# Performance work log

Measured on AMD Instinct MI355X. Metric: run time of the kernel, lower is better.

The kernel has to match this reference:

```python
import jax, jax.numpy as jnp
import numpy as np
from jax import lax

BITWIDTH = 7
EPS = 1e-5


def ti_quant(x):
    """TiFloatToInt8: per-tensor int8 quantization with power-of-2 scale."""
    rng = jnp.max(jnp.abs(x))
    bw = jnp.ceil(jnp.log2(rng))
    exp = bw - BITWIDTH
    q = jnp.clip(jnp.round(x * 2.0 ** (BITWIDTH - bw)), -128.0, 127.0)
    return q, exp


def ti_conv(xv, xe, wv, we, pad):
    """TiConv2d: integer conv (simulated in f32, all values int-valued),
    int32 accumulate, then shift back to 8 bits; exponents add."""
    acc = lax.conv_general_dilated(
        xv, wv, window_strides=(1, 1), padding=[(pad, pad), (pad, pad)],
        dimension_numbers=("NCHW", "OIHW", "NCHW"))
    rng = jnp.max(jnp.abs(acc))
    bw = jnp.ceil(jnp.log2(rng))
    shift = jnp.maximum(bw - BITWIDTH, 0.0)
    q = jnp.clip(jnp.round(acc * 2.0 ** (-shift)), -128.0, 127.0)
    return q, xe + we + shift


def batchnorm(x, gamma, beta):
    # training-mode BN: batch statistics over (N, H, W)
    mean = jnp.mean(x, axis=(0, 2, 3), keepdims=True)
    var = jnp.var(x, axis=(0, 2, 3), keepdims=True)
    g = gamma[None, :, None, None]
    b = beta[None, :, None, None]
    return g * (x - mean) * lax.rsqrt(var + EPS) + b


def setup_inputs() -> dict:
    key = jax.random.key(0)
    k0, k1, k2, k3, k4 = jax.random.split(key, 5)
    B, Cin, Cout, H, W = 32, 128, 256, 56, 56
    x_val = jax.random.randint(k0, (B, Cin, H, W), -128, 128, dtype=jnp.int32)
    x_exp = jnp.zeros((), jnp.float32) - 7.0
    wDW = jnp.round(jnp.clip(jax.random.normal(k1, (Cin, Cin, 3, 3), jnp.float32) * 32.0, -128.0, 127.0))
    wDW_exp = jnp.zeros((), jnp.float32) - 9.0
    wPW = jnp.round(jnp.clip(jax.random.normal(k2, (Cout, Cin, 1, 1), jnp.float32) * 32.0, -128.0, 127.0))
    wPW_exp = jnp.zeros((), jnp.float32) - 9.0
    gamma1 = jnp.ones((Cin,), jnp.float32) + 0.1 * jax.random.normal(k3, (Cin,), jnp.float32)
    beta1 = jnp.zeros((Cin,), jnp.float32)
    gamma2 = jnp.ones((Cout,), jnp.float32) + 0.1 * jax.random.normal(k4, (Cout,), jnp.float32)
    beta2 = jnp.zeros((Cout,), jnp.float32)
    return {"x_val": x_val, "x_exp": x_exp, "wDW": wDW, "wDW_exp": wDW_exp,
            "wPW": wPW, "wPW_exp": wPW_exp, "gamma1": gamma1, "beta1": beta1,
            "gamma2": gamma2, "beta2": beta2}


def reference(x_val, x_exp, wDW, wDW_exp, wPW, wPW_exp, gamma1, beta1, gamma2, beta2):
    xv = x_val.astype(jnp.float32)
    # convDW (3x3, in->in, pad=1)
    q, e = ti_conv(xv, x_exp, wDW, wDW_exp, 1)
    # dequant -> bn1 -> quant
    f = batchnorm(q * 2.0 ** e, gamma1, beta1)
    q, e = ti_quant(f)
    # TiReLU on int values
    q = jnp.maximum(q, 0.0)
    # convPW (1x1, in->out)
    q, e = ti_conv(q, e, wPW, wPW_exp, 0)
    # dequant -> bn2 -> quant -> relu
    f = batchnorm(q * 2.0 ** e, gamma2, beta2)
    q, e = ti_quant(f)
    q = jnp.maximum(q, 0.0)
    return q.astype(jnp.int8), e
```

## Files before the change

### kernel.cpp

```cpp
#include <hip/hip_runtime.h>
#include <cstdint>
#include <cstddef>

#define C1 128
#define C2 256
#define Hh 56
#define Wd 56
#define HW 3136
#define NHW 100352
#define N1 ((size_t)12845056)
#define N2 ((size_t)25690112)
#define XPSZ ((size_t)13778944)

typedef int v4i __attribute__((ext_vector_type(4)));
typedef int v16i __attribute__((ext_vector_type(16)));

static constexpr size_t OFF_XP = 0;
static constexpr size_t OFF_ACC1 = XPSZ;
static constexpr size_t OFF_Q1 = OFF_ACC1 + 4 * N1;
static constexpr size_t OFF_Q3 = OFF_Q1 + N1;
static constexpr size_t OFF_WQ1 = OFF_Q3 + N2;
static constexpr size_t OFF_WQ2 = OFF_WQ1 + 147456;
static constexpr size_t OFF_STATS = OFF_WQ2 + 32768;

struct Stats {
  int absmax1, absmax2, pad0, pad1;
  float scale1, e1, s2, e2;
  float scaleq2, e3, sf, ef;
  int sum1[C1]; unsigned sumsq1[C1];
  int min1[C1], max1[C1];
  float A1[C1], B1c[C1];
  int sum2[C2]; unsigned sumsq2[C2];
  int min2[C2], max2[C2];
  float A2[C2], B2c[C2];
};

__global__ void k_init(Stats* st) {
  int t = threadIdx.x;
  if (t == 0) { st->absmax1 = 0; st->absmax2 = 0; }
  for (int c = t; c < C1; c += 256) {
    st->sum1[c] = 0; st->sumsq1[c] = 0; st->min1[c] = 127; st->max1[c] = -128;
  }
  for (int c = t; c < C2; c += 256) {
    st->sum2[c] = 0; st->sumsq2[c] = 0; st->min2[c] = 127; st->max2[c] = -128;
  }
}

__global__ __launch_bounds__(256) void k_prep_x2(
    const int* __restrict__ x, signed char* __restrict__ xp) {
  __shared__ signed char lds[56 * 132];
  int t = threadIdx.x;
  int hh = blockIdx.x;
  int n = blockIdx.y;
  int* xpw = (int*)(xp + ((size_t)n * 58 + hh) * 7424);
  if (hh == 0 || hh == 57) {
    for (int o = t; o < 1856; o += 256) xpw[o] = 0;
    return;
  }
  int h = hh - 1;
  const int* xb = x + (size_t)n * C1 * HW + h * 56;
  for (int idx = t; idx < 7168; idx += 256) {
    int c = idx / 56, w = idx - c * 56;
    lds[w * 132 + c] = (signed char)xb[(size_t)c * HW + w];
  }
  __syncthreads();
  for (int o = t; o < 1856; o += 256) {
    int kb = o / 232, r = o - kb * 232, ww = r >> 2, cw = r & 3;
    int val = (ww == 0 || ww == 57) ? 0
              : *(const int*)&lds[(ww - 1) * 132 + kb * 16 + cw * 4];
    xpw[o] = val;
  }
}

__global__ void k_prep_w1(const float* __restrict__ wDW, signed char* __restrict__ wq1t) {
  int idx = blockIdx.x * 256 + threadIdx.x;
  if (idx >= 128 * 1152) return;
  int co = idx / 1152, r = idx - co * 1152;
  int ci = r / 9, pos = r - ci * 9;
  int k = pos * 128 + ci;
  wq1t[(size_t)(k >> 4) * 2048 + co * 16 + (k & 15)] = (signed char)(int)wDW[idx];
}

__global__ void k_prep_w2(const float* __restrict__ wPW, signed char* __restrict__ wq2t) {
  int i = blockIdx.x * 256 + threadIdx.x;
  int co = i >> 7, ci = i & 127;
  wq2t[(size_t)(ci >> 4) * 4096 + co * 16 + (ci & 15)] = (signed char)(int)wPW[i];
}

__device__ inline v4i ld16_lds(const signed char* p) {
  const int2* q = (const int2*)p;
  int2 lo = q[0], hi = q[1];
  v4i r; r[0] = lo.x; r[1] = lo.y; r[2] = hi.x; r[3] = hi.y;
  return r;
}

__global__ __launch_bounds__(256, 2) void k_conv1s(
    const signed char* __restrict__ xp, const signed char* __restrict__ wq1t,
    int* __restrict__ acc1, Stats* st) {
  __shared__ int reda[4];
  int t = threadIdx.x, lane = t & 63, wave = t >> 6;
  int half = lane >> 5, l31 = lane & 31;
  size_t g0 = (size_t)blockIdx.x * 256;

  const signed char* ab[2];
#pragma unroll
  for (int i = 0; i < 2; ++i) {
    size_t gm = g0 + wave * 64 + i * 32 + l31;
    int n = (int)(gm / HW);
    int p = (int)(gm - (size_t)n * HW);
    int h = p / 56, w = p - h * 56;
    ab[i] = xp + ((size_t)n * 58 + h) * 7424 + w * 16 + half * 928;
  }
  const signed char* bb[4];
#pragma unroll
  for (int j = 0; j < 4; ++j)
    bb[j] = wq1t + (size_t)(j * 32 + l31) * 16 + half * 2048;

  v16i a1[2][4];
#pragma unroll
  for (int i = 0; i < 2; ++i)
#pragma unroll
    for (int j = 0; j < 4; ++j)
#pragma unroll
      for (int r = 0; r < 16; ++r) a1[i][j][r] = 0;

#pragma unroll
  for (int pos = 0; pos < 9; ++pos) {
    int kh = pos / 3, kw = pos - kh * 3;
    const signed char* a0p = ab[0] + kh * 7424 + kw * 16;
    const signed char* a1p = ab[1] + kh * 7424 + kw * 16;
#pragma unroll
    for (int kb = 0; kb < 8; kb += 2) {
      v4i af0 = *(const v4i*)(a0p + kb * 928);
      v4i af1 = *(const v4i*)(a1p + kb * 928);
      v4i bf[4];
#pragma unroll
      for (int j = 0; j < 4; ++j)
        bf[j] = *(const v4i*)(bb[j] + pos * 16384 + kb * 2048);
#pragma unroll
      for (int j = 0; j < 4; ++j) {
        a1[0][j] = __builtin_amdgcn_mfma_i32_32x32x32_i8(af0, bf[j], a1[0][j], 0, 0, 0);
        a1[1][j] = __builtin_amdgcn_mfma_i32_32x32x32_i8(af1, bf[j], a1[1][j], 0, 0, 0);
      }
    }
  }

  int am = 0;
#pragma unroll
  for (int i = 0; i < 2; ++i)
#pragma unroll
    for (int j = 0; j < 4; ++j)
#pragma unroll
      for (int r = 0; r < 16; ++r) am = max(am, abs(a1[i][j][r]));
  for (int off = 32; off; off >>= 1) am = max(am, __shfl_down(am, off, 64));
  if (lane == 0) reda[wave] = am;
  __syncthreads();
  if (t == 0)
    atomicMax(&st->absmax1, max(max(reda[0], reda[1]), max(reda[2], reda[3])));

  int* ob = acc1 + (size_t)blockIdx.x * 32768;
#pragma unroll
  for (int i = 0; i < 2; ++i)
#pragma unroll
    for (int j = 0; j < 4; ++j)
#pragma unroll
      for (int reg = 0; reg < 16; ++reg)
        ob[(((wave * 2 + i) * 4 + j) * 16 + reg) * 64 + lane] = a1[i][j][reg];
}

__global__ __launch_bounds__(256, 2) void k_qstats1(
    const int* __restrict__ acc1, signed char* __restrict__ q1, Stats* st,
    const float* __restrict__ x_exp, const float* __restrict__ wDW_exp) {
  __shared__ int qti[256 * 34];
  __shared__ int psum[C1], psq[C1], pmn[C1], pmx[C1];
  signed char* qt = (signed char*)qti;
  int t = threadIdx.x, lane = t & 63, wave = t >> 6;
  int half = lane >> 5, l31 = lane & 31;

  if (t < C1) { psum[t] = 0; psq[t] = 0; pmn[t] = 127; pmx[t] = -128; }
  __syncthreads();

  int v1 = st->absmax1;
  int pw = 31 - __clz(v1 | 1);
  int bw = ((v1 & (v1 - 1)) == 0) ? pw : pw + 1;
  int sh = max(bw - 7, 0);
  float scale1 = exp2f((float)(-sh));
  if (blockIdx.x == 0 && t == 0)
    st->e1 = x_exp[0] + wDW_exp[0] + (float)sh;

  const int* ib = acc1 + (size_t)blockIdx.x * 32768;
#pragma unroll
  for (int j = 0; j < 4; ++j) {
    int sj = 0, sqj = 0, mnj = 127, mxj = -128;
    int c = j * 32 + l31;
#pragma unroll
    for (int i = 0; i < 2; ++i)
#pragma unroll
      for (int reg = 0; reg < 16; ++reg) {
        int av = ib[(((wave * 2 + i) * 4 + j) * 16 + reg) * 64 + lane];
        int row = (reg & 3) + 8 * (reg >> 2) + 4 * half;
        int pix = wave * 64 + i * 32 + row;
        float r = rintf((float)av * scale1);
        r = fminf(fmaxf(r, -128.f), 127.f);
        int qi = (int)r;
        qt[pix * 136 + c] = (signed char)qi;
        sj += qi; sqj += qi * qi; mnj = min(mnj, qi); mxj = max(mxj, qi);
      }
    sj += __shfl_down(sj, 32, 64);
    sqj += __shfl_down(sqj, 32, 64);
    mnj = min(mnj, __shfl_down(mnj, 32, 64));
    mxj = max(mxj, __shfl_down(mxj, 32, 64));
    if (half == 0) {
      atomicAdd(&psum[c], sj); atomicAdd(&psq[c], sqj);
      atomicMin(&pmn[c], mnj); atomicMax(&pmx[c], mxj);
    }
  }
  __syncthreads();
  if (t < C1) {
    atomicAdd(&st->sum1[t], psum[t]);
    atomicAdd(&st->sumsq1[t], (unsigned)psq[t]);
    atomicMin(&st->min1[t], pmn[t]);
    atomicMax(&st->max1[t], pmx[t]);
  }
  int* q1w = (int*)(q1 + (size_t)blockIdx.x * 256 * 128);
  for (int idx = t; idx < 8192; idx += 256) {
    int pix = idx >> 5, c4 = idx & 31;
    q1w[idx] = qti[pix * 34 + c4];
  }
}

template <int STORE>
__global__ __launch_bounds__(256, 2) void k_conv2t(
    const signed char* __restrict__ q1, const signed char* __restrict__ wq2t,
    signed char* __restrict__ q3, Stats* st, const float* __restrict__ wPW_exp) {
  __shared__ int qti[128 * 34];
  __shared__ signed char stg[128 * 264];
  __shared__ int psum[C2], psq[C2], pmn[C2], pmx[C2];
  __shared__ int reda[4];
  signed char* qt = (signed char*)qti;

  int t = threadIdx.x, lane = t & 63, wave = t >> 6;
  int half = lane >> 5, l31 = lane & 31;
  size_t g0 = (size_t)blockIdx.x * 128;

  if (STORE) { psum[t] = 0; psq[t] = 0; pmn[t] = 127; pmx[t] = -128; }

  int c4 = t & 31;
  float Av[4], Bv[4];
#pragma unroll
  for (int jj = 0; jj < 4; ++jj) {
    Av[jj] = st->A1[c4 * 4 + jj];
    Bv[jj] = st->B1c[c4 * 4 + jj];
  }
  float s2 = st->s2;
  const int* q1w = (const int*)(q1 + g0 * 128);
#pragma unroll
  for (int k = 0; k < 16; ++k) {
    int idx = k * 256 + t;
    int v = q1w[idx];
    int pix = idx >> 5;
    int outv = 0;
#pragma unroll
    for (int jj = 0; jj < 4; ++jj) {
      int b = (signed char)(v >> (8 * jj));
      float y = Av[jj] * (float)b + Bv[jj];
      float r = rintf(y * s2);
      r = fminf(fmaxf(r, -128.f), 127.f);
      r = fmaxf(r, 0.f);
      outv |= ((int)r & 0xff) << (8 * jj);
    }
    qti[pix * 34 + c4] = outv;
  }
  __syncthreads();

  v16i acc[8];
#pragma unroll
  for (int j = 0; j < 8; ++j)
#pragma unroll
    for (int r = 0; r < 16; ++r) acc[j][r] = 0;

#pragma unroll
  for (int ks = 0; ks < 4; ++ks) {
    v4i af = ld16_lds(&qt[(wave * 32 + l31) * 136 + half * 16 + ks * 32]);
#pragma unroll
    for (int j = 0; j < 8; ++j) {
      v4i bf = *(const v4i*)(wq2t + (size_t)(ks * 2 + half) * 4096 + (j * 32 + l31) * 16);
      acc[j] = __builtin_amdgcn_mfma_i32_32x32x32_i8(af, bf, acc[j], 0, 0, 0);
    }
  }

  if (STORE == 0) {
    int am2 = 0;
#pragma unroll
    for (int j = 0; j < 8; ++j)
#pragma unroll
      for (int r = 0; r < 16; ++r) am2 = max(am2, abs(acc[j][r]));
    for (int off = 32; off; off >>= 1) am2 = max(am2, __shfl_down(am2, off, 64));
    if (lane == 0) reda[wave] = am2;
    __syncthreads();
    if (t == 0)
      atomicMax(&st->absmax2, max(max(reda[0], reda[1]), max(reda[2], reda[3])));
  } else {
    int v2 = st->absmax2;
    int pw = 31 - __clz(v2 | 1);
    int bw = ((v2 & (v2 - 1)) == 0) ? pw : pw + 1;
    int sh2 = max(bw - 7, 0);
    float scale2 = exp2f((float)(-sh2));
    if (blockIdx.x == 0 && t == 0)
      st->e3 = st->e2 + wPW_exp[0] + (float)sh2;
#pragma unroll
    for (int j = 0; j < 8; ++j) {
      int c = j * 32 + l31;
      int sj = 0, sqj = 0, mnj = 127, mxj = -128;
#pragma unroll
      for (int reg = 0; reg < 16; ++reg) {
        int row = (reg & 3) + 8 * (reg >> 2) + 4 * half;
        float r = rintf((float)acc[j][reg] * scale2);
        r = fminf(fmaxf(r, -128.f), 127.f);
        int qi = (int)r;
        stg[(wave * 32 + row) * 264 + c] = (signed char)qi;
        sj += qi; sqj += qi * qi; mnj = min(mnj, qi); mxj = max(mxj, qi);
      }
      sj += __shfl_down(sj, 32, 64);
      sqj += __shfl_down(sqj, 32, 64);
      mnj = min(mnj, __shfl_down(mnj, 32, 64));
      mxj = max(mxj, __shfl_down(mxj, 32, 64));
      if (half == 0) {
        atomicAdd(&psum[c], sj); atomicAdd(&psq[c], sqj);
        atomicMin(&pmn[c], mnj); atomicMax(&pmx[c], mxj);
      }
    }
    __syncthreads();
    atomicAdd(&st->sum2[t], psum[t]);
    atomicAdd(&st->sumsq2[t], (unsigned)psq[t]);
    atomicMin(&st->min2[t], pmn[t]);
    atomicMax(&st->max2[t], pmx[t]);
    int* q3w = (int*)(q3 + g0 * 256);
#pragma unroll
    for (int k = 0; k < 32; ++k) {
      int idx = k * 256 + t;
      int pix = idx >> 6, cw = idx & 63;
      q3w[idx] = *(const int*)&stg[pix * 264 + cw * 4];
    }
  }
}

__global__ void k_bn(const int* __restrict__ sums,
                     const unsigned* __restrict__ sumsqs,
                     const int* __restrict__ mins, const int* __restrict__ maxs,
                     const float* __restrict__ gamma, const float* __restrict__ beta,
                     const float* __restrict__ e_in,
                     float* A, float* Bc, float* s_out, float* e_out,
                     float* e_extra, int C) {
  __shared__ float red[4];
  int t = threadIdx.x;
  float e1 = *e_in;
  double meanq = (double)sums[t] / (double)NHW;
  double varq = (double)sumsqs[t] / (double)NHW - meanq * meanq;
  float se = exp2f(e1);
  float mean = (float)meanq * se;
  float var = (float)varq * se * se;
  float rsq = 1.0f / sqrtf(var + 1e-5f);
  float g = gamma[t], b = beta[t];
  float Avv = g * se * rsq;
  float Bvv = b - g * mean * rsq;
  A[t] = Avv; Bc[t] = Bvv;
  float cand = fmaxf(fabsf(Avv * (float)mins[t] + Bvv), fabsf(Avv * (float)maxs[t] + Bvv));
  for (int off = 32; off; off >>= 1) cand = fmaxf(cand, __shfl_down(cand, off, 64));
  int wave = t >> 6, lane = t & 63;
  if (lane == 0) red[wave] = cand;
  __syncthreads();
  if (t == 0) {
    float rng = red[0];
    for (int i = 1; i < C / 64; i++) rng = fmaxf(rng, red[i]);
    float bwv = ceilf(log2f(rng));
    *s_out = exp2f(7.0f - bwv);
    *e_out = bwv - 7.0f;
    if (e_extra) *e_extra = bwv - 7.0f;
  }
}

__global__ __launch_bounds__(256) void k_out(
    const signed char* __restrict__ q3, const Stats* __restrict__ st,
    float* __restrict__ out) {
  __shared__ signed char lds[64 * 260];
  int t = threadIdx.x, lane = t & 63, wave = t >> 6;
  size_t g0 = (size_t)blockIdx.x * 64;
  int n = (int)(g0 / HW), p0 = (int)(g0 - (size_t)n * HW);
  const int* q3w = (const int*)(q3 + g0 * 256);
#pragma unroll
  for (int k = 0; k < 16; ++k) {
    int idx = k * 256 + t;
    int pix = idx >> 6, cw = idx & 63;
    *(int*)&lds[pix * 260 + cw * 4] = q3w[idx];
  }
  __syncthreads();
  float sf = st->sf;
  float* ob = out + (size_t)n * C2 * HW + p0 + lane;
#pragma unroll
  for (int cg = 0; cg < 16; ++cg) {
    int v = *(const int*)&lds[lane * 260 + wave * 64 + cg * 4];
#pragma unroll
    for (int jj = 0; jj < 4; ++jj) {
      int c = wave * 64 + cg * 4 + jj;
      float y = st->A2[c] * (float)((signed char)(v >> (8 * jj))) + st->B2c[c];
      float r = rintf(y * sf);
      r = fminf(fmaxf(r, -128.f), 127.f);
      ob[(size_t)c * HW] = fmaxf(r, 0.f);
    }
  }
}

extern "C" void kernel_launch(void* const* d_in, const int* in_sizes, int n_in,
                              void* d_out, int out_size, void* d_ws, size_t ws_size,
                              hipStream_t stream) {
  const int* x = (const int*)d_in[0];
  const float* x_exp = (const float*)d_in[1];
  const float* wDW = (const float*)d_in[2];
  const float* wDW_exp = (const float*)d_in[3];
  const float* wPW = (const float*)d_in[4];
  const float* wPW_exp = (const float*)d_in[5];
  const float* gamma1 = (const float*)d_in[6];
  const float* beta1 = (const float*)d_in[7];
  const float* gamma2 = (const float*)d_in[8];
  const float* beta2 = (const float*)d_in[9];
  float* out = (float*)d_out;

  char* ws = (char*)d_ws;
  signed char* xp2 = (signed char*)(ws + OFF_XP);
  int* acc1 = (int*)(ws + OFF_ACC1);
  signed char* q1 = (signed char*)(ws + OFF_Q1);
  signed char* q3 = (signed char*)(ws + OFF_Q3);
  signed char* wq1t = (signed char*)(ws + OFF_WQ1);
  signed char* wq2t = (signed char*)(ws + OFF_WQ2);
  Stats* st = (Stats*)(ws + OFF_STATS);

  hipLaunchKernelGGL(k_init, dim3(1), dim3(256), 0, stream, st);
  hipLaunchKernelGGL(k_prep_x2, dim3(58, 32), dim3(256), 0, stream, x, xp2);
  hipLaunchKernelGGL(k_prep_w1, dim3(576), dim3(256), 0, stream, wDW, wq1t);
  hipLaunchKernelGGL(k_prep_w2, dim3(128), dim3(256), 0, stream, wPW, wq2t);

  hipLaunchKernelGGL(k_conv1s, dim3(392), dim3(256), 0, stream,
                     xp2, wq1t, acc1, st);
  hipLaunchKernelGGL(k_qstats1, dim3(392), dim3(256), 0, stream,
                     acc1, q1, st, x_exp, wDW_exp);
  hipLaunchKernelGGL(k_bn, dim3(1), dim3(C1), 0, stream,
                     st->sum1, st->sumsq1, st->min1, st->max1, gamma1, beta1,
                     &st->e1, st->A1, st->B1c, &st->s2, &st->e2, (float*)nullptr, C1);

  hipLaunchKernelGGL(k_conv2t<0>, dim3(784), dim3(256), 0, stream,
                     q1, wq2t, q3, st, wPW_exp);
  hipLaunchKernelGGL(k_conv2t<1>, dim3(784), dim3(256), 0, stream,
                     q1, wq2t, q3, st, wPW_exp);
  hipLaunchKernelGGL(k_bn, dim3(1), dim3(C2), 0, stream,
                     st->sum2, st->sumsq2, st->min2, st->max2, gamma2, beta2,
                     &st->e3, st->A2, st->B2c, &st->sf, &st->ef, out + N2, C2);
  hipLaunchKernelGGL(k_out, dim3(1568), dim3(256), 0, stream, q3, st, out);
}
```

Measured before the change: 297.7 us.

## Fold BN-parameter kernels into consumers, merge prep kernels, halve conv1 tiles

```diff
diff --git a/kernel.cpp b/kernel.cpp
--- a/kernel.cpp
+++ b/kernel.cpp
@@ -29,20 +29,32 @@
   float scaleq2, e3, sf, ef;
   int sum1[C1]; unsigned sumsq1[C1];
   int min1[C1], max1[C1];
-  float A1[C1], B1c[C1];
   int sum2[C2]; unsigned sumsq2[C2];
   int min2[C2], max2[C2];
-  float A2[C2], B2c[C2];
 };
 
-__global__ void k_init(Stats* st) {
-  int t = threadIdx.x;
-  if (t == 0) { st->absmax1 = 0; st->absmax2 = 0; }
-  for (int c = t; c < C1; c += 256) {
-    st->sum1[c] = 0; st->sumsq1[c] = 0; st->min1[c] = 127; st->max1[c] = -128;
-  }
-  for (int c = t; c < C2; c += 256) {
-    st->sum2[c] = 0; st->sumsq2[c] = 0; st->min2[c] = 127; st->max2[c] = -128;
+__global__ __launch_bounds__(256) void k_prep_all(
+    const float* __restrict__ wDW, const float* __restrict__ wPW,
+    signed char* __restrict__ wq1t, signed char* __restrict__ wq2t, Stats* st) {
+  int b = blockIdx.x, t = threadIdx.x;
+  if (b < 576) {
+    int idx = b * 256 + t;
+    int co = idx / 1152, r = idx - co * 1152;
+    int ci = r / 9, pos = r - ci * 9;
+    int k = pos * 128 + ci;
+    wq1t[(size_t)(k >> 4) * 2048 + co * 16 + (k & 15)] = (signed char)(int)wDW[idx];
+  } else if (b < 704) {
+    int i = (b - 576) * 256 + t;
+    int co = i >> 7, ci = i & 127;
+    wq2t[(size_t)(ci >> 4) * 4096 + co * 16 + (ci & 15)] = (signed char)(int)wPW[i];
+  } else {
+    if (t == 0) { st->absmax1 = 0; st->absmax2 = 0; }
+    for (int c = t; c < C1; c += 256) {
+      st->sum1[c] = 0; st->sumsq1[c] = 0; st->min1[c] = 127; st->max1[c] = -128;
+    }
+    for (int c = t; c < C2; c += 256) {
+      st->sum2[c] = 0; st->sumsq2[c] = 0; st->min2[c] = 127; st->max2[c] = -128;
+    }
   }
 }
 
@@ -72,21 +84,6 @@
   }
 }
 
-__global__ void k_prep_w1(const float* __restrict__ wDW, signed char* __restrict__ wq1t) {
-  int idx = blockIdx.x * 256 + threadIdx.x;
-  if (idx >= 128 * 1152) return;
-  int co = idx / 1152, r = idx - co * 1152;
-  int ci = r / 9, pos = r - ci * 9;
-  int k = pos * 128 + ci;
-  wq1t[(size_t)(k >> 4) * 2048 + co * 16 + (k & 15)] = (signed char)(int)wDW[idx];
-}
-
-__global__ void k_prep_w2(const float* __restrict__ wPW, signed char* __restrict__ wq2t) {
-  int i = blockIdx.x * 256 + threadIdx.x;
-  int co = i >> 7, ci = i & 127;
-  wq2t[(size_t)(ci >> 4) * 4096 + co * 16 + (ci & 15)] = (signed char)(int)wPW[i];
-}
-
 __device__ inline v4i ld16_lds(const signed char* p) {
   const int2* q = (const int2*)p;
   int2 lo = q[0], hi = q[1];
@@ -94,33 +91,34 @@
   return r;
 }
 
-__global__ __launch_bounds__(256, 2) void k_conv1s(
+__global__ __launch_bounds__(256, 4) void k_conv1s(
     const signed char* __restrict__ xp, const signed char* __restrict__ wq1t,
     int* __restrict__ acc1, Stats* st) {
   __shared__ int reda[4];
   int t = threadIdx.x, lane = t & 63, wave = t >> 6;
   int half = lane >> 5, l31 = lane & 31;
-  size_t g0 = (size_t)blockIdx.x * 256;
+  int mw = wave & 1, nw = wave >> 1;
+  size_t g0 = (size_t)blockIdx.x * 128;
 
   const signed char* ab[2];
 #pragma unroll
   for (int i = 0; i < 2; ++i) {
-    size_t gm = g0 + wave * 64 + i * 32 + l31;
+    size_t gm = g0 + mw * 64 + i * 32 + l31;
     int n = (int)(gm / HW);
     int p = (int)(gm - (size_t)n * HW);
     int h = p / 56, w = p - h * 56;
     ab[i] = xp + ((size_t)n * 58 + h) * 7424 + w * 16 + half * 928;
   }
-  const signed char* bb[4];
-#pragma unroll
-  for (int j = 0; j < 4; ++j)
-    bb[j] = wq1t + (size_t)(j * 32 + l31) * 16 + half * 2048;
-
-  v16i a1[2][4];
+  const signed char* bb[2];
+#pragma unroll
+  for (int j = 0; j < 2; ++j)
+    bb[j] = wq1t + (size_t)(nw * 64 + j * 32 + l31) * 16 + half * 2048;
+
+  v16i a1[2][2];
 #pragma unroll
   for (int i = 0; i < 2; ++i)
 #pragma unroll
-    for (int j = 0; j < 4; ++j)
+    for (int j = 0; j < 2; ++j)
 #pragma unroll
       for (int r = 0; r < 16; ++r) a1[i][j][r] = 0;
 
@@ -133,15 +131,12 @@
     for (int kb = 0; kb < 8; kb += 2) {
       v4i af0 = *(const v4i*)(a0p + kb * 928);
       v4i af1 = *(const v4i*)(a1p + kb * 928);
-      v4i bf[4];
-#pragma unroll
-      for (int j = 0; j < 4; ++j)
-        bf[j] = *(const v4i*)(bb[j] + pos * 16384 + kb * 2048);
-#pragma unroll
-      for (int j = 0; j < 4; ++j) {
-        a1[0][j] = __builtin_amdgcn_mfma_i32_32x32x32_i8(af0, bf[j], a1[0][j], 0, 0, 0);
-        a1[1][j] = __builtin_amdgcn_mfma_i32_32x32x32_i8(af1, bf[j], a1[1][j], 0, 0, 0);
-      }
+      v4i bf0 = *(const v4i*)(bb[0] + pos * 16384 + kb * 2048);
+      v4i bf1 = *(const v4i*)(bb[1] + pos * 16384 + kb * 2048);
+      a1[0][0] = __builtin_amdgcn_mfma_i32_32x32x32_i8(af0, bf0, a1[0][0], 0, 0, 0);
+      a1[0][1] = __builtin_amdgcn_mfma_i32_32x32x32_i8(af0, bf1, a1[0][1], 0, 0, 0);
+      a1[1][0] = __builtin_amdgcn_mfma_i32_32x32x32_i8(af1, bf0, a1[1][0], 0, 0, 0);
+      a1[1][1] = __builtin_amdgcn_mfma_i32_32x32x32_i8(af1, bf1, a1[1][1], 0, 0, 0);
     }
   }
 
@@ -149,7 +144,7 @@
 #pragma unroll
   for (int i = 0; i < 2; ++i)
 #pragma unroll
-    for (int j = 0; j < 4; ++j)
+    for (int j = 0; j < 2; ++j)
 #pragma unroll
       for (int r = 0; r < 16; ++r) am = max(am, abs(a1[i][j][r]));
   for (int off = 32; off; off >>= 1) am = max(am, __shfl_down(am, off, 64));
@@ -158,24 +153,25 @@
   if (t == 0)
     atomicMax(&st->absmax1, max(max(reda[0], reda[1]), max(reda[2], reda[3])));
 
-  int* ob = acc1 + (size_t)blockIdx.x * 32768;
+  int* ob = acc1 + (size_t)blockIdx.x * 16384;
 #pragma unroll
   for (int i = 0; i < 2; ++i)
 #pragma unroll
-    for (int j = 0; j < 4; ++j)
+    for (int j = 0; j < 2; ++j)
 #pragma unroll
       for (int reg = 0; reg < 16; ++reg)
-        ob[(((wave * 2 + i) * 4 + j) * 16 + reg) * 64 + lane] = a1[i][j][reg];
-}
-
-__global__ __launch_bounds__(256, 2) void k_qstats1(
+        ob[(((wave * 2 + i) * 2 + j) * 16 + reg) * 64 + lane] = a1[i][j][reg];
+}
+
+__global__ __launch_bounds__(256, 4) void k_qstats1(
     const int* __restrict__ acc1, signed char* __restrict__ q1, Stats* st,
     const float* __restrict__ x_exp, const float* __restrict__ wDW_exp) {
-  __shared__ int qti[256 * 34];
+  __shared__ int qti[128 * 34];
   __shared__ int psum[C1], psq[C1], pmn[C1], pmx[C1];
   signed char* qt = (signed char*)qti;
   int t = threadIdx.x, lane = t & 63, wave = t >> 6;
   int half = lane >> 5, l31 = lane & 31;
+  int mw = wave & 1, nw = wave >> 1;
 
   if (t < C1) { psum[t] = 0; psq[t] = 0; pmn[t] = 127; pmx[t] = -128; }
   __syncthreads();
@@ -188,18 +184,18 @@
   if (blockIdx.x == 0 && t == 0)
     st->e1 = x_exp[0] + wDW_exp[0] + (float)sh;
 
-  const int* ib = acc1 + (size_t)blockIdx.x * 32768;
-#pragma unroll
-  for (int j = 0; j < 4; ++j) {
+  const int* ib = acc1 + (size_t)blockIdx.x * 16384;
+#pragma unroll
+  for (int j = 0; j < 2; ++j) {
     int sj = 0, sqj = 0, mnj = 127, mxj = -128;
-    int c = j * 32 + l31;
+    int c = nw * 64 + j * 32 + l31;
 #pragma unroll
     for (int i = 0; i < 2; ++i)
 #pragma unroll
       for (int reg = 0; reg < 16; ++reg) {
-        int av = ib[(((wave * 2 + i) * 4 + j) * 16 + reg) * 64 + lane];
+        int av = ib[(((wave * 2 + i) * 2 + j) * 16 + reg) * 64 + lane];
         int row = (reg & 3) + 8 * (reg >> 2) + 4 * half;
-        int pix = wave * 64 + i * 32 + row;
+        int pix = mw * 64 + i * 32 + row;
         float r = rintf((float)av * scale1);
         r = fminf(fmaxf(r, -128.f), 127.f);
         int qi = (int)r;
@@ -222,22 +218,25 @@
     atomicMin(&st->min1[t], pmn[t]);
     atomicMax(&st->max1[t], pmx[t]);
   }
-  int* q1w = (int*)(q1 + (size_t)blockIdx.x * 256 * 128);
-  for (int idx = t; idx < 8192; idx += 256) {
+  int* q1w = (int*)(q1 + (size_t)blockIdx.x * 128 * 128);
+  for (int idx = t; idx < 4096; idx += 256) {
     int pix = idx >> 5, c4 = idx & 31;
     q1w[idx] = qti[pix * 34 + c4];
   }
 }
 
 template <int STORE>
-__global__ __launch_bounds__(256, 2) void k_conv2t(
+__global__ __launch_bounds__(256, 4) void k_conv2t(
     const signed char* __restrict__ q1, const signed char* __restrict__ wq2t,
-    signed char* __restrict__ q3, Stats* st, const float* __restrict__ wPW_exp) {
-  __shared__ int qti[128 * 34];
-  __shared__ signed char stg[128 * 264];
+    signed char* __restrict__ q3, Stats* st,
+    const float* __restrict__ gamma1, const float* __restrict__ beta1,
+    const float* __restrict__ wPW_exp) {
+  __shared__ int bufi[8448];
   __shared__ int psum[C2], psq[C2], pmn[C2], pmx[C2];
+  __shared__ float bnA[C1], bnB[C1], redf[2];
   __shared__ int reda[4];
-  signed char* qt = (signed char*)qti;
+  signed char* qt = (signed char*)bufi;
+  signed char* stg = (signed char*)bufi;
 
   int t = threadIdx.x, lane = t & 63, wave = t >> 6;
   int half = lane >> 5, l31 = lane & 31;
@@ -245,14 +244,39 @@
 
   if (STORE) { psum[t] = 0; psq[t] = 0; pmn[t] = 127; pmx[t] = -128; }
 
+  float e1 = st->e1;
+  float cand = 0.f;
+  if (t < C1) {
+    double meanq = (double)st->sum1[t] / (double)NHW;
+    double varq = (double)st->sumsq1[t] / (double)NHW - meanq * meanq;
+    float se = exp2f(e1);
+    float mean = (float)meanq * se;
+    float var = (float)varq * se * se;
+    float rsq = 1.0f / sqrtf(var + 1e-5f);
+    float g = gamma1[t], b = beta1[t];
+    float Avv = g * se * rsq;
+    float Bvv = b - g * mean * rsq;
+    bnA[t] = Avv; bnB[t] = Bvv;
+    cand = fmaxf(fabsf(Avv * (float)st->min1[t] + Bvv),
+                 fabsf(Avv * (float)st->max1[t] + Bvv));
+  }
+  if (wave < 2) {
+    for (int off = 32; off; off >>= 1) cand = fmaxf(cand, __shfl_down(cand, off, 64));
+    if (lane == 0) redf[wave] = cand;
+  }
+  __syncthreads();
+  float rng = fmaxf(redf[0], redf[1]);
+  float bwv = ceilf(log2f(rng));
+  float s2 = exp2f(7.0f - bwv);
+  float e2 = bwv - 7.0f;
+
   int c4 = t & 31;
   float Av[4], Bv[4];
 #pragma unroll
   for (int jj = 0; jj < 4; ++jj) {
-    Av[jj] = st->A1[c4 * 4 + jj];
-    Bv[jj] = st->B1c[c4 * 4 + jj];
-  }
-  float s2 = st->s2;
+    Av[jj] = bnA[c4 * 4 + jj];
+    Bv[jj] = bnB[c4 * 4 + jj];
+  }
   const int* q1w = (const int*)(q1 + g0 * 128);
 #pragma unroll
   for (int k = 0; k < 16; ++k) {
@@ -269,67 +293,95 @@
       r = fmaxf(r, 0.f);
       outv |= ((int)r & 0xff) << (8 * jj);
     }
-    qti[pix * 34 + c4] = outv;
-  }
-  __syncthreads();
-
-  v16i acc[8];
-#pragma unroll
-  for (int j = 0; j < 8; ++j)
-#pragma unroll
-    for (int r = 0; r < 16; ++r) acc[j][r] = 0;
-
-#pragma unroll
-  for (int ks = 0; ks < 4; ++ks) {
-    v4i af = ld16_lds(&qt[(wave * 32 + l31) * 136 + half * 16 + ks * 32]);
-#pragma unroll
-    for (int j = 0; j < 8; ++j) {
-      v4i bf = *(const v4i*)(wq2t + (size_t)(ks * 2 + half) * 4096 + (j * 32 + l31) * 16);
-      acc[j] = __builtin_amdgcn_mfma_i32_32x32x32_i8(af, bf, acc[j], 0, 0, 0);
+    bufi[pix * 34 + c4] = outv;
+  }
+  __syncthreads();
+
+  int am2 = 0;
+  float scale2 = 0.f;
+  int sh2 = 0;
+  if (STORE) {
+    int v2 = st->absmax2;
+    int pw = 31 - __clz(v2 | 1);
+    int bw = ((v2 & (v2 - 1)) == 0) ? pw : pw + 1;
+    sh2 = max(bw - 7, 0);
+    scale2 = exp2f((float)(-sh2));
+    if (blockIdx.x == 0 && t == 0)
+      st->e3 = e2 + wPW_exp[0] + (float)sh2;
+  }
+  int pq[2][4][4];
+#pragma unroll
+  for (int ch = 0; ch < 2; ++ch) {
+    v16i acc[4];
+#pragma unroll
+    for (int j = 0; j < 4; ++j)
+#pragma unroll
+      for (int r = 0; r < 16; ++r) acc[j][r] = 0;
+#pragma unroll
+    for (int ks = 0; ks < 4; ++ks) {
+      v4i af = ld16_lds(&qt[(wave * 32 + l31) * 136 + half * 16 + ks * 32]);
+#pragma unroll
+      for (int j = 0; j < 4; ++j) {
+        v4i bf = *(const v4i*)(wq2t + (size_t)(ks * 2 + half) * 4096 +
+                               (ch * 128 + j * 32 + l31) * 16);
+        acc[j] = __builtin_amdgcn_mfma_i32_32x32x32_i8(af, bf, acc[j], 0, 0, 0);
+      }
+    }
+    if (STORE == 0) {
+#pragma unroll
+      for (int j = 0; j < 4; ++j)
+#pragma unroll
+        for (int r = 0; r < 16; ++r) am2 = max(am2, abs(acc[j][r]));
+    } else {
+#pragma unroll
+      for (int j = 0; j < 4; ++j) {
+        int c = ch * 128 + j * 32 + l31;
+        int sj = 0, sqj = 0, mnj = 127, mxj = -128;
+        int pk[4] = {0, 0, 0, 0};
+#pragma unroll
+        for (int reg = 0; reg < 16; ++reg) {
+          float r = rintf((float)acc[j][reg] * scale2);
+          r = fminf(fmaxf(r, -128.f), 127.f);
+          int qi = (int)r;
+          pk[reg >> 2] |= (qi & 0xff) << ((reg & 3) * 8);
+          sj += qi; sqj += qi * qi; mnj = min(mnj, qi); mxj = max(mxj, qi);
+        }
+#pragma unroll
+        for (int k = 0; k < 4; ++k) pq[ch][j][k] = pk[k];
+        sj += __shfl_down(sj, 32, 64);
+        sqj += __shfl_down(sqj, 32, 64);
+        mnj = min(mnj, __shfl_down(mnj, 32, 64));
+        mxj = max(mxj, __shfl_down(mxj, 32, 64));
+        if (half == 0) {
+          atomicAdd(&psum[c], sj); atomicAdd(&psq[c], sqj);
+          atomicMin(&pmn[c], mnj); atomicMax(&pmx[c], mxj);
+        }
+      }
     }
   }
 
   if (STORE == 0) {
-    int am2 = 0;
-#pragma unroll
-    for (int j = 0; j < 8; ++j)
-#pragma unroll
-      for (int r = 0; r < 16; ++r) am2 = max(am2, abs(acc[j][r]));
     for (int off = 32; off; off >>= 1) am2 = max(am2, __shfl_down(am2, off, 64));
     if (lane == 0) reda[wave] = am2;
     __syncthreads();
     if (t == 0)
       atomicMax(&st->absmax2, max(max(reda[0], reda[1]), max(reda[2], reda[3])));
   } else {
-    int v2 = st->absmax2;
-    int pw = 31 - __clz(v2 | 1);
-    int bw = ((v2 & (v2 - 1)) == 0) ? pw : pw + 1;
-    int sh2 = max(bw - 7, 0);
-    float scale2 = exp2f((float)(-sh2));
-    if (blockIdx.x == 0 && t == 0)
-      st->e3 = st->e2 + wPW_exp[0] + (float)sh2;
-#pragma unroll
-    for (int j = 0; j < 8; ++j) {
-      int c = j * 32 + l31;
-      int sj = 0, sqj = 0, mnj = 127, mxj = -128;
-#pragma unroll
-      for (int reg = 0; reg < 16; ++reg) {
-        int row = (reg & 3) + 8 * (reg >> 2) + 4 * half;
-        float r = rintf((float)acc[j][reg] * scale2);
-        r = fminf(fmaxf(r, -128.f), 127.f);
-        int qi = (int)r;
-        stg[(wave * 32 + row) * 264 + c] = (signed char)qi;
-        sj += qi; sqj += qi * qi; mnj = min(mnj, qi); mxj = max(mxj, qi);
-      }
-      sj += __shfl_down(sj, 32, 64);
-      sqj += __shfl_down(sqj, 32, 64);
-      mnj = min(mnj, __shfl_down(mnj, 32, 64));
-      mxj = max(mxj, __shfl_down(mxj, 32, 64));
-      if (half == 0) {
-        atomicAdd(&psum[c], sj); atomicAdd(&psq[c], sqj);
-        atomicMin(&pmn[c], mnj); atomicMax(&pmx[c], mxj);
-      }
-    }
+    __syncthreads();
+#pragma unroll
+    for (int ch = 0; ch < 2; ++ch)
+#pragma unroll
+      for (int j = 0; j < 4; ++j)
+#pragma unroll
+        for (int k = 0; k < 4; ++k) {
+          int word = pq[ch][j][k];
+#pragma unroll
+          for (int b = 0; b < 4; ++b) {
+            int row = b + 8 * k + 4 * half;
+            stg[(wave * 32 + row) * 264 + ch * 128 + j * 32 + l31] =
+                (signed char)(word >> (8 * b));
+          }
+        }
     __syncthreads();
     atomicAdd(&st->sum2[t], psum[t]);
     atomicAdd(&st->sumsq2[t], (unsigned)psq[t]);
@@ -345,45 +397,12 @@
   }
 }
 
-__global__ void k_bn(const int* __restrict__ sums,
-                     const unsigned* __restrict__ sumsqs,
-                     const int* __restrict__ mins, const int* __restrict__ maxs,
-                     const float* __restrict__ gamma, const float* __restrict__ beta,
-                     const float* __restrict__ e_in,
-                     float* A, float* Bc, float* s_out, float* e_out,
-                     float* e_extra, int C) {
-  __shared__ float red[4];
-  int t = threadIdx.x;
-  float e1 = *e_in;
-  double meanq = (double)sums[t] / (double)NHW;
-  double varq = (double)sumsqs[t] / (double)NHW - meanq * meanq;
-  float se = exp2f(e1);
-  float mean = (float)meanq * se;
-  float var = (float)varq * se * se;
-  float rsq = 1.0f / sqrtf(var + 1e-5f);
-  float g = gamma[t], b = beta[t];
-  float Avv = g * se * rsq;
-  float Bvv = b - g * mean * rsq;
-  A[t] = Avv; Bc[t] = Bvv;
-  float cand = fmaxf(fabsf(Avv * (float)mins[t] + Bvv), fabsf(Avv * (float)maxs[t] + Bvv));
-  for (int off = 32; off; off >>= 1) cand = fmaxf(cand, __shfl_down(cand, off, 64));
-  int wave = t >> 6, lane = t & 63;
-  if (lane == 0) red[wave] = cand;
-  __syncthreads();
-  if (t == 0) {
-    float rng = red[0];
-    for (int i = 1; i < C / 64; i++) rng = fmaxf(rng, red[i]);
-    float bwv = ceilf(log2f(rng));
-    *s_out = exp2f(7.0f - bwv);
-    *e_out = bwv - 7.0f;
-    if (e_extra) *e_extra = bwv - 7.0f;
-  }
-}
-
 __global__ __launch_bounds__(256) void k_out(
     const signed char* __restrict__ q3, const Stats* __restrict__ st,
+    const float* __restrict__ gamma2, const float* __restrict__ beta2,
     float* __restrict__ out) {
   __shared__ signed char lds[64 * 260];
+  __shared__ float bnA2[C2], bnB2[C2], redf2[4];
   int t = threadIdx.x, lane = t & 63, wave = t >> 6;
   size_t g0 = (size_t)blockIdx.x * 64;
   int n = (int)(g0 / HW), p0 = (int)(g0 - (size_t)n * HW);
@@ -394,8 +413,29 @@
     int pix = idx >> 6, cw = idx & 63;
     *(int*)&lds[pix * 260 + cw * 4] = q3w[idx];
   }
-  __syncthreads();
-  float sf = st->sf;
+  float e3 = st->e3;
+  {
+    double meanq = (double)st->sum2[t] / (double)NHW;
+    double varq = (double)st->sumsq2[t] / (double)NHW - meanq * meanq;
+    float se = exp2f(e3);
+    float mean = (float)meanq * se;
+    float var = (float)varq * se * se;
+    float rsq = 1.0f / sqrtf(var + 1e-5f);
+    float g = gamma2[t], b = beta2[t];
+    float Avv = g * se * rsq;
+    float Bvv = b - g * mean * rsq;
+    bnA2[t] = Avv; bnB2[t] = Bvv;
+    float cand = fmaxf(fabsf(Avv * (float)st->min2[t] + Bvv),
+                       fabsf(Avv * (float)st->max2[t] + Bvv));
+    for (int off = 32; off; off >>= 1) cand = fmaxf(cand, __shfl_down(cand, off, 64));
+    if (lane == 0) redf2[wave] = cand;
+  }
+  __syncthreads();
+  float rng = fmaxf(fmaxf(redf2[0], redf2[1]), fmaxf(redf2[2], redf2[3]));
+  float bwv = ceilf(log2f(rng));
+  float sf = exp2f(7.0f - bwv);
+  if (blockIdx.x == 0 && t == 0) out[N2] = bwv - 7.0f;
+
   float* ob = out + (size_t)n * C2 * HW + p0 + lane;
 #pragma unroll
   for (int cg = 0; cg < 16; ++cg) {
@@ -403,7 +443,7 @@
 #pragma unroll
     for (int jj = 0; jj < 4; ++jj) {
       int c = wave * 64 + cg * 4 + jj;
-      float y = st->A2[c] * (float)((signed char)(v >> (8 * jj))) + st->B2c[c];
+      float y = bnA2[c] * (float)((signed char)(v >> (8 * jj))) + bnB2[c];
       float r = rintf(y * sf);
       r = fminf(fmaxf(r, -128.f), 127.f);
       ob[(size_t)c * HW] = fmaxf(r, 0.f);
@@ -435,25 +475,20 @@
   signed char* wq2t = (signed char*)(ws + OFF_WQ2);
   Stats* st = (Stats*)(ws + OFF_STATS);
 
-  hipLaunchKernelGGL(k_init, dim3(1), dim3(256), 0, stream, st);
+  hipLaunchKernelGGL(k_prep_all, dim3(705), dim3(256), 0, stream,
+                     wDW, wPW, wq1t, wq2t, st);
   hipLaunchKernelGGL(k_prep_x2, dim3(58, 32), dim3(256), 0, stream, x, xp2);
-  hipLaunchKernelGGL(k_prep_w1, dim3(576), dim3(256), 0, stream, wDW, wq1t);
-  hipLaunchKernelGGL(k_prep_w2, dim3(128), dim3(256), 0, stream, wPW, wq2t);
-
-  hipLaunchKernelGGL(k_conv1s, dim3(392), dim3(256), 0, stream,
+
+  hipLaunchKernelGGL(k_conv1s, dim3(784), dim3(256), 0, stream,
                      xp2, wq1t, acc1, st);
-  hipLaunchKernelGGL(k_qstats1, dim3(392), dim3(256), 0, stream,
+  hipLaunchKernelGGL(k_qstats1, dim3(784), dim3(256), 0, stream,
                      acc1, q1, st, x_exp, wDW_exp);
-  hipLaunchKernelGGL(k_bn, dim3(1), dim3(C1), 0, stream,
-                     st->sum1, st->sumsq1, st->min1, st->max1, gamma1, beta1,
-                     &st->e1, st->A1, st->B1c, &st->s2, &st->e2, (float*)nullptr, C1);
 
   hipLaunchKernelGGL(k_conv2t<0>, dim3(784), dim3(256), 0, stream,
-                     q1, wq2t, q3, st, wPW_exp);
+                     q1, wq2t, q3, st, gamma1, beta1, wPW_exp);
   hipLaunchKernelGGL(k_conv2t<1>, dim3(784), dim3(256), 0, stream,
-                     q1, wq2t, q3, st, wPW_exp);
-  hipLaunchKernelGGL(k_bn, dim3(1), dim3(C2), 0, stream,
-                     st->sum2, st->sumsq2, st->min2, st->max2, gamma2, beta2,
-                     &st->e3, st->A2, st->B2c, &st->sf, &st->ef, out + N2, C2);
-  hipLaunchKernelGGL(k_out, dim3(1568), dim3(256), 0, stream, q3, st, out);
-}
+                     q1, wq2t, q3, st, gamma1, beta1, wPW_exp);
+
+  hipLaunchKernelGGL(k_out, dim3(1568), dim3(256), 0, stream,
+                     q3, st, gamma2, beta2, out);
+}
```

Result: slower. 316.4 us (+6.3%).
